# Kernel optimization log

Measured on AMD Instinct MI355X. Metric: run time of the kernel, lower is better.

## Reference

```python
import jax, jax.numpy as jnp
import numpy as np

B, T, C, H = 2, 2048, 1024, 16
D = C // H  # head dim = 64
EPS = 1e-5


def setup_inputs() -> dict:
    key = jax.random.key(0)
    k1, k2, k3 = jax.random.split(key, 3)
    x = jax.random.normal(k1, (B, T, C), dtype=jnp.float32)
    W_attn = jax.random.normal(k2, (3 * C, C), dtype=jnp.float32) * 0.02
    W_proj = jax.random.normal(k3, (C, C), dtype=jnp.float32) * 0.02
    # standard RoPE inverse frequencies, one per rotation pair (D//2)
    rope_freqs = 1.0 / (10000.0 ** (jnp.arange(D // 2, dtype=jnp.float32) * 2.0 / D))
    ln_weight = jnp.ones((C,), dtype=jnp.float32)
    ln_bias = jnp.zeros((C,), dtype=jnp.float32)
    return {"x": x, "rope_freqs": rope_freqs, "W_attn": W_attn,
            "W_proj": W_proj, "ln_weight": ln_weight, "ln_bias": ln_bias}


def _apply_rope(q, k, freqs):
    # q,k: [B,H,S,D]; matches torch apply_rope: split even/odd, concat halves
    S = q.shape[-2]
    theta = jnp.arange(S, dtype=q.dtype)[:, None] * freqs[None, :]  # [S, D/2]
    sin_t, cos_t = jnp.sin(theta), jnp.cos(theta)

    def rot(t):
        t1, t2 = t[..., 0::2], t[..., 1::2]
        return jnp.concatenate([t1 * cos_t - t2 * sin_t,
                                t1 * sin_t + t2 * cos_t], axis=-1)

    return rot(q), rot(k)


def reference(x, rope_freqs, W_attn, W_proj, ln_weight, ln_bias):
    Bv, Tv, Cv = x.shape
    qkv = x @ W_attn.T                      # [B,T,3C] (F.linear, no bias)
    q, k, v = jnp.split(qkv, 3, axis=-1)
    resh = lambda t: t.reshape(Bv, Tv, H, D).transpose(0, 2, 1, 3)  # [B,H,T,D]
    q, k, v = resh(q), resh(k), resh(v)
    q, k = _apply_rope(q, k, rope_freqs)
    scale = 1.0 / jnp.sqrt(jnp.asarray(D, dtype=x.dtype))
    scores = jnp.einsum('bhqd,bhkd->bhqk', q, k) * scale
    causal = jnp.tril(jnp.ones((Tv, Tv), dtype=bool))
    scores = jnp.where(causal[None, None], scores, -jnp.inf)
    att = jax.nn.softmax(scores, axis=-1)
    y = jnp.einsum('bhqk,bhkd->bhqd', att, v)
    y = y.transpose(0, 2, 1, 3).reshape(Bv, Tv, Cv)
    y = y @ W_proj.T                        # c_proj (bias=False)
    # resid dropout is identity in eval; LayerNorm (eps=1e-5, biased var)
    mean = jnp.mean(y, axis=-1, keepdims=True)
    var = jnp.mean(jnp.square(y - mean), axis=-1, keepdims=True)
    return (y - mean) / jnp.sqrt(var + EPS) * ln_weight + ln_bias
```

## Files before the change

### kernel.cpp

```cpp
#include <hip/hip_runtime.h>
#include <hip/hip_bf16.h>
#include <math.h>

typedef short bf16x8 __attribute__((ext_vector_type(8)));
typedef float f32x4 __attribute__((ext_vector_type(4)));

#define T_SEQ 2048
#define C_DIM 1024
#define H_HEADS 16
#define D_HEAD 64
#define BT 4096
#define C3 3072
#define BH 32

static __device__ inline unsigned short bf_bits(float f) {
    __hip_bfloat16 h = __float2bfloat16(f);
    unsigned short u;
    __builtin_memcpy(&u, &h, 2);
    return u;
}

static __device__ inline unsigned int cvtpk(float lo, float hi) {
    unsigned int r;
    asm("v_cvt_pk_bf16_f32 %0, %1, %2" : "=v"(r) : "v"(lo), "v"(hi));
    return r;
}

__device__ __forceinline__ void gload16(const void* g, void* l) {
    __builtin_amdgcn_global_load_lds(
        (const __attribute__((address_space(1))) void*)g,
        (__attribute__((address_space(3))) void*)l, 16, 0, 0);
}

__device__ __forceinline__ int swz(int r) {
    return ((((r & 3) ^ ((r >> 3) & 3)) | (((r >> 3) & 1) << 2)) << 3);
}

__global__ void cast_f32_bf16(const float* __restrict__ in,
                              __hip_bfloat16* __restrict__ out, int n4) {
    int i = blockIdx.x * blockDim.x + threadIdx.x;
    if (i >= n4) return;
    float4 v = reinterpret_cast<const float4*>(in)[i];
    ushort4 o;
    o.x = bf_bits(v.x); o.y = bf_bits(v.y); o.z = bf_bits(v.z); o.w = bf_bits(v.w);
    reinterpret_cast<ushort4*>(out)[i] = o;
}

__global__ void rope_table(const float* __restrict__ freqs, float2* __restrict__ tab) {
    int idx = blockIdx.x * 256 + threadIdx.x;
    int i = idx & 31, tp = idx >> 5;
    float th = (float)tp * freqs[i];
    tab[idx] = make_float2(cosf(th), sinf(th));
}

template<int MODE, int BN>
__global__ __launch_bounds__(256) void gemm_bt(
    const __hip_bfloat16* __restrict__ A,
    const __hip_bfloat16* __restrict__ Bw,
    void* __restrict__ Cout, int M, int N, int K,
    const float2* __restrict__ tab,
    __hip_bfloat16* __restrict__ q_s,
    __hip_bfloat16* __restrict__ k_s,
    __hip_bfloat16* __restrict__ v_t) {
    __shared__ __hip_bfloat16 As[128][64];
    __shared__ __hip_bfloat16 Bs[BN][64];
    const int t = threadIdx.x;
    const int lane = t & 63, w = t >> 6;
    const int wr = w >> 1, wc = w & 1;
    const int l15 = lane & 15, lg = lane >> 4;
    const int m0 = blockIdx.y * 128, n0 = blockIdx.x * BN;

    const int srow = lane >> 3;
    const int scol = ((lane & 7) ^ srow) * 8;
    const int xr = (l15 & 7) << 3;

    constexpr int NF = BN / 32;
    f32x4 acc[4][NF];
    f32x4 zero4 = {0.f, 0.f, 0.f, 0.f};
#pragma unroll
    for (int m = 0; m < 4; m++)
#pragma unroll
        for (int n = 0; n < NF; n++) acc[m][n] = zero4;

    const int nt = K >> 6;
    for (int tk = 0; tk < nt; tk++) {
        const int k0 = tk << 6;
#pragma unroll
        for (int i = 0; i < 4; i++) {
            int rbase = w * 32 + i * 8;
            gload16(&A[(size_t)(m0 + rbase + srow) * K + k0 + scol], &As[rbase][0]);
        }
#pragma unroll
        for (int i = 0; i < NF; i++) {
            int rbase = w * (BN / 4) + i * 8;
            gload16(&Bw[(size_t)(n0 + rbase + srow) * K + k0 + scol], &Bs[rbase][0]);
        }
        __syncthreads();
#pragma unroll
        for (int kk = 0; kk < 2; kk++) {
            bf16x8 a[4], b[NF];
            const int co = (kk * 32 + lg * 8) ^ xr;
#pragma unroll
            for (int m = 0; m < 4; m++)
                a[m] = *reinterpret_cast<const bf16x8*>(&As[wr * 64 + m * 16 + l15][co]);
#pragma unroll
            for (int n = 0; n < NF; n++)
                b[n] = *reinterpret_cast<const bf16x8*>(&Bs[wc * (BN / 2) + n * 16 + l15][co]);
            __builtin_amdgcn_s_setprio(1);
#pragma unroll
            for (int m = 0; m < 4; m++)
#pragma unroll
                for (int n = 0; n < NF; n++)
                    acc[m][n] = __builtin_amdgcn_mfma_f32_16x16x32_bf16(a[m], b[n], acc[m][n], 0, 0, 0);
            __builtin_amdgcn_s_setprio(0);
        }
        __syncthreads();
    }

    if (MODE == 2) {
        const int region = n0 >> 10;
#pragma unroll
        for (int m = 0; m < 4; m++)
#pragma unroll
            for (int n = 0; n < NF; n++) {
                const int col = n0 + wc * (BN / 2) + n * 16 + l15;
                const int d = col & 63;
                const int h = (col >> 6) & 15;
                const int row0 = m0 + wr * 64 + m * 16 + lg * 4;
                const int b = row0 >> 11;
                const int tp0 = row0 & 2047;
                if (region < 2) {
                    const int i = d >> 1, odd = d & 1;
                    const int dp = (d >> 1) + (odd ? 32 : 0);
                    __hip_bfloat16* dst = (region == 0) ? q_s : k_s;
                    const float sc = (region == 0) ? 0.125f * 1.44269504f : 1.0f;
#pragma unroll
                    for (int jj = 0; jj < 4; jj++) {
                        float own = acc[m][n][jj];
                        float par = __shfl_xor(own, 1);
                        float2 cs = tab[(tp0 + jj) * 32 + i];
                        float val = own * cs.x + (odd ? par : -par) * cs.y;
                        dst[((size_t)(b * H_HEADS + h) * T_SEQ + tp0 + jj) * D_HEAD + dp] =
                            __float2bfloat16(val * sc);
                    }
                } else {
                    ushort4 ov;
                    ov.x = bf_bits(acc[m][n][0]);
                    ov.y = bf_bits(acc[m][n][1]);
                    ov.z = bf_bits(acc[m][n][2]);
                    ov.w = bf_bits(acc[m][n][3]);
                    *reinterpret_cast<ushort4*>(
                        &v_t[((size_t)(b * H_HEADS + h) * D_HEAD + d) * T_SEQ + tp0]) = ov;
                }
            }
        return;
    }

#pragma unroll
    for (int m = 0; m < 4; m++)
#pragma unroll
        for (int n = 0; n < NF; n++)
#pragma unroll
            for (int jj = 0; jj < 4; jj++) {
                int row = m0 + wr * 64 + m * 16 + lg * 4 + jj;
                int col = n0 + wc * (BN / 2) + n * 16 + l15;
                float v = acc[m][n][jj];
                if (MODE == 1)
                    ((__hip_bfloat16*)Cout)[(size_t)row * N + col] = __float2bfloat16(v);
                else
                    ((float*)Cout)[(size_t)row * N + col] = v;
            }
}

__global__ __launch_bounds__(256, 4) void attn_kernel(
    const __hip_bfloat16* __restrict__ q_s,
    const __hip_bfloat16* __restrict__ k_s,
    const __hip_bfloat16* __restrict__ v_t,
    __hip_bfloat16* __restrict__ y) {
    __shared__ ushort Kbuf[2][64 * 64];
    __shared__ ushort Vbuf[2][64 * 64];

    const int bid = blockIdx.x;
    const int qt = 31 - (bid >> 5);
    const int bh = bid & 31;
    const int t = threadIdx.x, lane = t & 63, w = t >> 6;
    const int l15 = lane & 15, lg = lane >> 4;
    const size_t hbase = (size_t)bh * T_SEQ * D_HEAD;
    const int qr = qt * 64 + w * 16 + l15;

    bf16x8 aq[2];
#pragma unroll
    for (int dd = 0; dd < 2; dd++)
        aq[dd] = *reinterpret_cast<const bf16x8*>(&q_s[hbase + (size_t)qr * 64 + dd * 32 + lg * 8]);

    bf16x8 ones;
#pragma unroll
    for (int i = 0; i < 8; i++) ones[i] = (short)0x3F80;

    f32x4 zero4 = {0.f, 0.f, 0.f, 0.f};
    f32x4 o[4];
#pragma unroll
    for (int dc = 0; dc < 4; dc++) o[dc] = zero4;
    f32x4 lacc = zero4;
    float mr = -INFINITY;

    int koff[4][2], voff[4][2];
#pragma unroll
    for (int c = 0; c < 4; c++) {
        int kro = ((c >> 1) << 5) + ((c & 1) << 2) + ((l15 >> 2) << 3) + (l15 & 3);
        int sz = swz(kro);
#pragma unroll
        for (int dd = 0; dd < 2; dd++)
            koff[c][dd] = kro * 64 + ((dd * 32 + lg * 8) ^ sz);
    }
#pragma unroll
    for (int dc = 0; dc < 4; dc++) {
        int vro = dc * 16 + l15;
        int sz = swz(vro);
#pragma unroll
        for (int dd = 0; dd < 2; dd++)
            voff[dc][dd] = vro * 64 + ((dd * 32 + lg * 8) ^ sz);
    }

    const int srow = t >> 3;
    const int sgr = t & 7;

    auto stageKV = [&](int buf, int kbase) {
#pragma unroll
        for (int i = 0; i < 2; i++) {
            int r = i * 32 + srow;
            int gsw = (sgr ^ (swz(r) >> 3)) * 8;
            gload16(&k_s[hbase + (size_t)(kbase + r) * 64 + gsw],
                    &Kbuf[buf][(i * 32 + w * 8) * 64]);
            gload16(&v_t[hbase + (size_t)r * T_SEQ + kbase + gsw],
                    &Vbuf[buf][(i * 32 + w * 8) * 64]);
        }
    };

    int cur = 0;
    stageKV(0, 0);
    __syncthreads();

    for (int kt = 0; kt <= qt; kt++) {
        const int kt64 = kt << 6;
        if (kt < qt) stageKV(cur ^ 1, kt64 + 64);

        const ushort* Kc = Kbuf[cur];
        const ushort* Vc = Vbuf[cur];
        bf16x8 kf[4][2], av[4][2];
#pragma unroll
        for (int c = 0; c < 4; c++)
#pragma unroll
            for (int dd = 0; dd < 2; dd++)
                kf[c][dd] = *reinterpret_cast<const bf16x8*>(&Kc[koff[c][dd]]);
#pragma unroll
        for (int dc = 0; dc < 4; dc++)
#pragma unroll
            for (int dd = 0; dd < 2; dd++)
                av[dc][dd] = *reinterpret_cast<const bf16x8*>(&Vc[voff[dc][dd]]);

        f32x4 st[4];
        __builtin_amdgcn_s_setprio(1);
#pragma unroll
        for (int c = 0; c < 4; c++) {
            st[c] = zero4;
#pragma unroll
            for (int dd = 0; dd < 2; dd++)
                st[c] = __builtin_amdgcn_mfma_f32_16x16x32_bf16(kf[c][dd], aq[dd], st[c], 0, 0, 0);
        }
        __builtin_amdgcn_s_setprio(0);

        if (kt == qt) {
#pragma unroll
            for (int c = 0; c < 4; c++) {
                int kb = kt64 + ((c >> 1) << 5) + ((c & 1) << 2) + lg * 8;
#pragma unroll
                for (int jj = 0; jj < 4; jj++)
                    if (kb + jj > qr) st[c][jj] = -INFINITY;
            }
        }

        float m0a = fmaxf(st[0][0], st[0][1]), m0b = fmaxf(st[0][2], st[0][3]);
        float m1a = fmaxf(st[1][0], st[1][1]), m1b = fmaxf(st[1][2], st[1][3]);
        float m2a = fmaxf(st[2][0], st[2][1]), m2b = fmaxf(st[2][2], st[2][3]);
        float m3a = fmaxf(st[3][0], st[3][1]), m3b = fmaxf(st[3][2], st[3][3]);
        float lmx = fmaxf(fmaxf(fmaxf(m0a, m0b), fmaxf(m1a, m1b)),
                          fmaxf(fmaxf(m2a, m2b), fmaxf(m3a, m3b)));

        if (__any(lmx - mr > 8.f)) {
            float mx = fmaxf(lmx, __shfl_xor(lmx, 16));
            mx = fmaxf(mx, __shfl_xor(mx, 32));
            float mnew = fmaxf(mr, mx);
            float scl = __builtin_amdgcn_exp2f(mr - mnew);
            mr = mnew;
            lacc[0] *= scl;
#pragma unroll
            for (int dc = 0; dc < 4; dc++)
#pragma unroll
                for (int jj = 0; jj < 4; jj++) o[dc][jj] *= scl;
        }

#pragma unroll
        for (int c = 0; c < 4; c++)
#pragma unroll
            for (int jj = 0; jj < 4; jj++)
                st[c][jj] = __builtin_amdgcn_exp2f(st[c][jj] - mr);

        union { bf16x8 v; unsigned int u[4]; } pf0, pf1;
        pf0.u[0] = cvtpk(st[0][0], st[0][1]);
        pf0.u[1] = cvtpk(st[0][2], st[0][3]);
        pf0.u[2] = cvtpk(st[1][0], st[1][1]);
        pf0.u[3] = cvtpk(st[1][2], st[1][3]);
        pf1.u[0] = cvtpk(st[2][0], st[2][1]);
        pf1.u[1] = cvtpk(st[2][2], st[2][3]);
        pf1.u[2] = cvtpk(st[3][0], st[3][1]);
        pf1.u[3] = cvtpk(st[3][2], st[3][3]);

        __builtin_amdgcn_s_setprio(1);
        lacc = __builtin_amdgcn_mfma_f32_16x16x32_bf16(ones, pf0.v, lacc, 0, 0, 0);
        lacc = __builtin_amdgcn_mfma_f32_16x16x32_bf16(ones, pf1.v, lacc, 0, 0, 0);
#pragma unroll
        for (int dc = 0; dc < 4; dc++) {
            o[dc] = __builtin_amdgcn_mfma_f32_16x16x32_bf16(av[dc][0], pf0.v, o[dc], 0, 0, 0);
            o[dc] = __builtin_amdgcn_mfma_f32_16x16x32_bf16(av[dc][1], pf1.v, o[dc], 0, 0, 0);
        }
        __builtin_amdgcn_s_setprio(0);

        __syncthreads();
        cur ^= 1;
    }

    const int b = bh >> 4, h = bh & 15;
    float inv = 1.f / lacc[0];
#pragma unroll
    for (int dc = 0; dc < 4; dc++) {
        ushort4 ov;
        ov.x = bf_bits(o[dc][0] * inv);
        ov.y = bf_bits(o[dc][1] * inv);
        ov.z = bf_bits(o[dc][2] * inv);
        ov.w = bf_bits(o[dc][3] * inv);
        *reinterpret_cast<ushort4*>(
            &y[(size_t)(b * T_SEQ + qr) * C_DIM + h * 64 + dc * 16 + lg * 4]) = ov;
    }
}

__global__ __launch_bounds__(256) void ln_kernel(const __hip_bfloat16* __restrict__ y2,
                                                 const float* __restrict__ wgt,
                                                 const float* __restrict__ bias,
                                                 float* __restrict__ out) {
    const int row = blockIdx.x;
    const int t = threadIdx.x;
    ushort4 u = reinterpret_cast<const ushort4*>(y2 + (size_t)row * C_DIM)[t];
    float4 v;
    v.x = __bfloat162float(*(__hip_bfloat16*)&u.x);
    v.y = __bfloat162float(*(__hip_bfloat16*)&u.y);
    v.z = __bfloat162float(*(__hip_bfloat16*)&u.z);
    v.w = __bfloat162float(*(__hip_bfloat16*)&u.w);
    float s = v.x + v.y + v.z + v.w;
    float s2 = v.x * v.x + v.y * v.y + v.z * v.z + v.w * v.w;
#pragma unroll
    for (int d = 1; d < 64; d <<= 1) {
        s += __shfl_xor(s, d);
        s2 += __shfl_xor(s2, d);
    }
    __shared__ float ps[4], ps2[4];
    const int lane = t & 63, w = t >> 6;
    if (lane == 0) { ps[w] = s; ps2[w] = s2; }
    __syncthreads();
    s = ps[0] + ps[1] + ps[2] + ps[3];
    s2 = ps2[0] + ps2[1] + ps2[2] + ps2[3];
    float mean = s * (1.f / C_DIM);
    float var = s2 * (1.f / C_DIM) - mean * mean;
    float inv = rsqrtf(var + 1e-5f);
    float4 wv = reinterpret_cast<const float4*>(wgt)[t];
    float4 bv = reinterpret_cast<const float4*>(bias)[t];
    float4 ov;
    ov.x = (v.x - mean) * inv * wv.x + bv.x;
    ov.y = (v.y - mean) * inv * wv.y + bv.y;
    ov.z = (v.z - mean) * inv * wv.z + bv.z;
    ov.w = (v.w - mean) * inv * wv.w + bv.w;
    reinterpret_cast<float4*>(out + (size_t)row * C_DIM)[t] = ov;
}

extern "C" void kernel_launch(void* const* d_in, const int* in_sizes, int n_in,
                              void* d_out, int out_size, void* d_ws, size_t ws_size,
                              hipStream_t stream) {
    const float* x      = (const float*)d_in[0];
    const float* freqs  = (const float*)d_in[1];
    const float* W_attn = (const float*)d_in[2];
    const float* W_proj = (const float*)d_in[3];
    const float* lnw    = (const float*)d_in[4];
    const float* lnb    = (const float*)d_in[5];
    float* out = (float*)d_out;
    char* ws = (char*)d_ws;

    __hip_bfloat16* xb   = (__hip_bfloat16*)(ws);
    __hip_bfloat16* Wab  = (__hip_bfloat16*)(ws + 8388608);
    __hip_bfloat16* Wpb  = (__hip_bfloat16*)(ws + 14680064);
    float2*         tab  = (float2*)(ws + 16777216);
    __hip_bfloat16* q_s  = (__hip_bfloat16*)(ws + 41943040);
    __hip_bfloat16* k_s  = (__hip_bfloat16*)(ws + 50331648);
    __hip_bfloat16* v_t  = (__hip_bfloat16*)(ws + 58720256);
    __hip_bfloat16* y_at = (__hip_bfloat16*)(ws + 67108864);
    __hip_bfloat16* y2b  = (__hip_bfloat16*)(ws + 75497472);

    rope_table<<<(T_SEQ * 32) / 256, 256, 0, stream>>>(freqs, tab);
    cast_f32_bf16<<<(BT * C_DIM / 4) / 256, 256, 0, stream>>>(x, xb, BT * C_DIM / 4);
    cast_f32_bf16<<<(C3 * C_DIM / 4) / 256, 256, 0, stream>>>(W_attn, Wab, C3 * C_DIM / 4);
    cast_f32_bf16<<<(C_DIM * C_DIM / 4) / 256, 256, 0, stream>>>(W_proj, Wpb, C_DIM * C_DIM / 4);

    gemm_bt<2, 128><<<dim3(C3 / 128, BT / 128), 256, 0, stream>>>(
        xb, Wab, nullptr, BT, C3, C_DIM, tab, q_s, k_s, v_t);

    attn_kernel<<<1024, 256, 0, stream>>>(q_s, k_s, v_t, y_at);

    gemm_bt<1, 64><<<dim3(C_DIM / 64, BT / 128), 256, 0, stream>>>(
        y_at, Wpb, y2b, BT, C_DIM, C_DIM, nullptr, nullptr, nullptr, nullptr);

    ln_kernel<<<BT, 256, 0, stream>>>(y2b, lnw, lnb, out);
}
```

Baseline: 112.5 us.

## Use 128-row query tiles in attention and fuse prep kernels into one launch

The attention kernel moves to 512-thread blocks covering 128 query rows, so eight waves share each staged K/V tile. Waves whose rows lie entirely before the current key tile skip its compute, and the causal mask is applied only on tiles that cross the diagonal. The four setup launches (three casts and the RoPE table) are merged into one prep kernel to cut launch overhead. The trade-off is causal load imbalance inside a block, since early-row waves idle while later waves work, plus half as many blocks to fill the GPU.

After: 112.6 us. Within noise of the previous version (+0.1%).

```diff
diff --git a/kernel.cpp b/kernel.cpp
--- a/kernel.cpp
+++ b/kernel.cpp
@@ -36,21 +36,32 @@
     return ((((r & 3) ^ ((r >> 3) & 3)) | (((r >> 3) & 1) << 2)) << 3);
 }
 
-__global__ void cast_f32_bf16(const float* __restrict__ in,
-                              __hip_bfloat16* __restrict__ out, int n4) {
-    int i = blockIdx.x * blockDim.x + threadIdx.x;
-    if (i >= n4) return;
-    float4 v = reinterpret_cast<const float4*>(in)[i];
-    ushort4 o;
-    o.x = bf_bits(v.x); o.y = bf_bits(v.y); o.z = bf_bits(v.z); o.w = bf_bits(v.w);
-    reinterpret_cast<ushort4*>(out)[i] = o;
-}
-
-__global__ void rope_table(const float* __restrict__ freqs, float2* __restrict__ tab) {
-    int idx = blockIdx.x * 256 + threadIdx.x;
-    int i = idx & 31, tp = idx >> 5;
-    float th = (float)tp * freqs[i];
-    tab[idx] = make_float2(cosf(th), sinf(th));
+__global__ void prep_kernel(const float* __restrict__ x,
+                            const float* __restrict__ Wa,
+                            const float* __restrict__ Wp,
+                            const float* __restrict__ freqs,
+                            __hip_bfloat16* __restrict__ xb,
+                            __hip_bfloat16* __restrict__ Wab,
+                            __hip_bfloat16* __restrict__ Wpb,
+                            float2* __restrict__ tab) {
+    const int bidx = blockIdx.x, tid = threadIdx.x;
+    if (bidx < 8192) {
+        const float* src;
+        __hip_bfloat16* dst;
+        int i;
+        if (bidx < 4096)      { src = x;  dst = xb;  i = bidx * 256 + tid; }
+        else if (bidx < 7168) { src = Wa; dst = Wab; i = (bidx - 4096) * 256 + tid; }
+        else                  { src = Wp; dst = Wpb; i = (bidx - 7168) * 256 + tid; }
+        float4 v = reinterpret_cast<const float4*>(src)[i];
+        ushort4 o;
+        o.x = bf_bits(v.x); o.y = bf_bits(v.y); o.z = bf_bits(v.z); o.w = bf_bits(v.w);
+        reinterpret_cast<ushort4*>(dst)[i] = o;
+    } else {
+        int idx = (bidx - 8192) * 256 + tid;
+        int i = idx & 31, tp = idx >> 5;
+        float th = (float)tp * freqs[i];
+        tab[idx] = make_float2(cosf(th), sinf(th));
+    }
 }
 
 template<int MODE, int BN>
@@ -164,15 +175,11 @@
             for (int jj = 0; jj < 4; jj++) {
                 int row = m0 + wr * 64 + m * 16 + lg * 4 + jj;
                 int col = n0 + wc * (BN / 2) + n * 16 + l15;
-                float v = acc[m][n][jj];
-                if (MODE == 1)
-                    ((__hip_bfloat16*)Cout)[(size_t)row * N + col] = __float2bfloat16(v);
-                else
-                    ((float*)Cout)[(size_t)row * N + col] = v;
-            }
-}
-
-__global__ __launch_bounds__(256, 4) void attn_kernel(
+                ((__hip_bfloat16*)Cout)[(size_t)row * N + col] = __float2bfloat16(acc[m][n][jj]);
+            }
+}
+
+__global__ __launch_bounds__(512, 4) void attn_kernel(
     const __hip_bfloat16* __restrict__ q_s,
     const __hip_bfloat16* __restrict__ k_s,
     const __hip_bfloat16* __restrict__ v_t,
@@ -181,12 +188,13 @@
     __shared__ ushort Vbuf[2][64 * 64];
 
     const int bid = blockIdx.x;
-    const int qt = 31 - (bid >> 5);
+    const int qt = 15 - (bid >> 5);
     const int bh = bid & 31;
     const int t = threadIdx.x, lane = t & 63, w = t >> 6;
     const int l15 = lane & 15, lg = lane >> 4;
     const size_t hbase = (size_t)bh * T_SEQ * D_HEAD;
-    const int qr = qt * 64 + w * 16 + l15;
+    const int qrow0 = qt * 128 + w * 16;
+    const int qr = qrow0 + l15;
 
     bf16x8 aq[2];
 #pragma unroll
@@ -224,107 +232,105 @@
 
     const int srow = t >> 3;
     const int sgr = t & 7;
+    const int gsw = (sgr ^ (swz(srow) >> 3)) * 8;
 
     auto stageKV = [&](int buf, int kbase) {
-#pragma unroll
-        for (int i = 0; i < 2; i++) {
-            int r = i * 32 + srow;
-            int gsw = (sgr ^ (swz(r) >> 3)) * 8;
-            gload16(&k_s[hbase + (size_t)(kbase + r) * 64 + gsw],
-                    &Kbuf[buf][(i * 32 + w * 8) * 64]);
-            gload16(&v_t[hbase + (size_t)r * T_SEQ + kbase + gsw],
-                    &Vbuf[buf][(i * 32 + w * 8) * 64]);
-        }
+        gload16(&k_s[hbase + (size_t)(kbase + srow) * 64 + gsw], &Kbuf[buf][(w * 8) * 64]);
+        gload16(&v_t[hbase + (size_t)srow * T_SEQ + kbase + gsw], &Vbuf[buf][(w * 8) * 64]);
     };
 
     int cur = 0;
     stageKV(0, 0);
     __syncthreads();
 
-    for (int kt = 0; kt <= qt; kt++) {
+    const int last = 2 * qt + 1;
+    for (int kt = 0; kt <= last; kt++) {
         const int kt64 = kt << 6;
-        if (kt < qt) stageKV(cur ^ 1, kt64 + 64);
-
-        const ushort* Kc = Kbuf[cur];
-        const ushort* Vc = Vbuf[cur];
-        bf16x8 kf[4][2], av[4][2];
-#pragma unroll
-        for (int c = 0; c < 4; c++)
-#pragma unroll
-            for (int dd = 0; dd < 2; dd++)
-                kf[c][dd] = *reinterpret_cast<const bf16x8*>(&Kc[koff[c][dd]]);
-#pragma unroll
-        for (int dc = 0; dc < 4; dc++)
-#pragma unroll
-            for (int dd = 0; dd < 2; dd++)
-                av[dc][dd] = *reinterpret_cast<const bf16x8*>(&Vc[voff[dc][dd]]);
-
-        f32x4 st[4];
-        __builtin_amdgcn_s_setprio(1);
-#pragma unroll
-        for (int c = 0; c < 4; c++) {
-            st[c] = zero4;
-#pragma unroll
-            for (int dd = 0; dd < 2; dd++)
-                st[c] = __builtin_amdgcn_mfma_f32_16x16x32_bf16(kf[c][dd], aq[dd], st[c], 0, 0, 0);
+        if (kt < last) stageKV(cur ^ 1, kt64 + 64);
+
+        const bool live = (kt64 <= qrow0 + 15);
+        if (live) {
+            const ushort* Kc = Kbuf[cur];
+            const ushort* Vc = Vbuf[cur];
+            bf16x8 kf[4][2], av[4][2];
+#pragma unroll
+            for (int c = 0; c < 4; c++)
+#pragma unroll
+                for (int dd = 0; dd < 2; dd++)
+                    kf[c][dd] = *reinterpret_cast<const bf16x8*>(&Kc[koff[c][dd]]);
+#pragma unroll
+            for (int dc = 0; dc < 4; dc++)
+#pragma unroll
+                for (int dd = 0; dd < 2; dd++)
+                    av[dc][dd] = *reinterpret_cast<const bf16x8*>(&Vc[voff[dc][dd]]);
+
+            f32x4 st[4];
+            __builtin_amdgcn_s_setprio(1);
+#pragma unroll
+            for (int c = 0; c < 4; c++) {
+                st[c] = zero4;
+#pragma unroll
+                for (int dd = 0; dd < 2; dd++)
+                    st[c] = __builtin_amdgcn_mfma_f32_16x16x32_bf16(kf[c][dd], aq[dd], st[c], 0, 0, 0);
+            }
+            __builtin_amdgcn_s_setprio(0);
+
+            if (kt64 + 63 > qrow0) {
+#pragma unroll
+                for (int c = 0; c < 4; c++) {
+                    int kb = kt64 + ((c >> 1) << 5) + ((c & 1) << 2) + lg * 8;
+#pragma unroll
+                    for (int jj = 0; jj < 4; jj++)
+                        if (kb + jj > qr) st[c][jj] = -INFINITY;
+                }
+            }
+
+            float m0a = fmaxf(st[0][0], st[0][1]), m0b = fmaxf(st[0][2], st[0][3]);
+            float m1a = fmaxf(st[1][0], st[1][1]), m1b = fmaxf(st[1][2], st[1][3]);
+            float m2a = fmaxf(st[2][0], st[2][1]), m2b = fmaxf(st[2][2], st[2][3]);
+            float m3a = fmaxf(st[3][0], st[3][1]), m3b = fmaxf(st[3][2], st[3][3]);
+            float lmx = fmaxf(fmaxf(fmaxf(m0a, m0b), fmaxf(m1a, m1b)),
+                              fmaxf(fmaxf(m2a, m2b), fmaxf(m3a, m3b)));
+
+            if (__any(lmx - mr > 8.f)) {
+                float mx = fmaxf(lmx, __shfl_xor(lmx, 16));
+                mx = fmaxf(mx, __shfl_xor(mx, 32));
+                float mnew = fmaxf(mr, mx);
+                float scl = __builtin_amdgcn_exp2f(mr - mnew);
+                mr = mnew;
+                lacc[0] *= scl;
+#pragma unroll
+                for (int dc = 0; dc < 4; dc++)
+#pragma unroll
+                    for (int jj = 0; jj < 4; jj++) o[dc][jj] *= scl;
+            }
+
+#pragma unroll
+            for (int c = 0; c < 4; c++)
+#pragma unroll
+                for (int jj = 0; jj < 4; jj++)
+                    st[c][jj] = __builtin_amdgcn_exp2f(st[c][jj] - mr);
+
+            union { bf16x8 v; unsigned int u[4]; } pf0, pf1;
+            pf0.u[0] = cvtpk(st[0][0], st[0][1]);
+            pf0.u[1] = cvtpk(st[0][2], st[0][3]);
+            pf0.u[2] = cvtpk(st[1][0], st[1][1]);
+            pf0.u[3] = cvtpk(st[1][2], st[1][3]);
+            pf1.u[0] = cvtpk(st[2][0], st[2][1]);
+            pf1.u[1] = cvtpk(st[2][2], st[2][3]);
+            pf1.u[2] = cvtpk(st[3][0], st[3][1]);
+            pf1.u[3] = cvtpk(st[3][2], st[3][3]);
+
+            __builtin_amdgcn_s_setprio(1);
+            lacc = __builtin_amdgcn_mfma_f32_16x16x32_bf16(ones, pf0.v, lacc, 0, 0, 0);
+            lacc = __builtin_amdgcn_mfma_f32_16x16x32_bf16(ones, pf1.v, lacc, 0, 0, 0);
+#pragma unroll
+            for (int dc = 0; dc < 4; dc++) {
+                o[dc] = __builtin_amdgcn_mfma_f32_16x16x32_bf16(av[dc][0], pf0.v, o[dc], 0, 0, 0);
+                o[dc] = __builtin_amdgcn_mfma_f32_16x16x32_bf16(av[dc][1], pf1.v, o[dc], 0, 0, 0);
+            }
+            __builtin_amdgcn_s_setprio(0);
         }
-        __builtin_amdgcn_s_setprio(0);
-
-        if (kt == qt) {
-#pragma unroll
-            for (int c = 0; c < 4; c++) {
-                int kb = kt64 + ((c >> 1) << 5) + ((c & 1) << 2) + lg * 8;
-#pragma unroll
-                for (int jj = 0; jj < 4; jj++)
-                    if (kb + jj > qr) st[c][jj] = -INFINITY;
-            }
-        }
-
-        float m0a = fmaxf(st[0][0], st[0][1]), m0b = fmaxf(st[0][2], st[0][3]);
-        float m1a = fmaxf(st[1][0], st[1][1]), m1b = fmaxf(st[1][2], st[1][3]);
-        float m2a = fmaxf(st[2][0], st[2][1]), m2b = fmaxf(st[2][2], st[2][3]);
-        float m3a = fmaxf(st[3][0], st[3][1]), m3b = fmaxf(st[3][2], st[3][3]);
-        float lmx = fmaxf(fmaxf(fmaxf(m0a, m0b), fmaxf(m1a, m1b)),
-                          fmaxf(fmaxf(m2a, m2b), fmaxf(m3a, m3b)));
-
-        if (__any(lmx - mr > 8.f)) {
-            float mx = fmaxf(lmx, __shfl_xor(lmx, 16));
-            mx = fmaxf(mx, __shfl_xor(mx, 32));
-            float mnew = fmaxf(mr, mx);
-            float scl = __builtin_amdgcn_exp2f(mr - mnew);
-            mr = mnew;
-            lacc[0] *= scl;
-#pragma unroll
-            for (int dc = 0; dc < 4; dc++)
-#pragma unroll
-                for (int jj = 0; jj < 4; jj++) o[dc][jj] *= scl;
-        }
-
-#pragma unroll
-        for (int c = 0; c < 4; c++)
-#pragma unroll
-            for (int jj = 0; jj < 4; jj++)
-                st[c][jj] = __builtin_amdgcn_exp2f(st[c][jj] - mr);
-
-        union { bf16x8 v; unsigned int u[4]; } pf0, pf1;
-        pf0.u[0] = cvtpk(st[0][0], st[0][1]);
-        pf0.u[1] = cvtpk(st[0][2], st[0][3]);
-        pf0.u[2] = cvtpk(st[1][0], st[1][1]);
-        pf0.u[3] = cvtpk(st[1][2], st[1][3]);
-        pf1.u[0] = cvtpk(st[2][0], st[2][1]);
-        pf1.u[1] = cvtpk(st[2][2], st[2][3]);
-        pf1.u[2] = cvtpk(st[3][0], st[3][1]);
-        pf1.u[3] = cvtpk(st[3][2], st[3][3]);
-
-        __builtin_amdgcn_s_setprio(1);
-        lacc = __builtin_amdgcn_mfma_f32_16x16x32_bf16(ones, pf0.v, lacc, 0, 0, 0);
-        lacc = __builtin_amdgcn_mfma_f32_16x16x32_bf16(ones, pf1.v, lacc, 0, 0, 0);
-#pragma unroll
-        for (int dc = 0; dc < 4; dc++) {
-            o[dc] = __builtin_amdgcn_mfma_f32_16x16x32_bf16(av[dc][0], pf0.v, o[dc], 0, 0, 0);
-            o[dc] = __builtin_amdgcn_mfma_f32_16x16x32_bf16(av[dc][1], pf1.v, o[dc], 0, 0, 0);
-        }
-        __builtin_amdgcn_s_setprio(0);
 
         __syncthreads();
         cur ^= 1;
@@ -404,15 +410,12 @@
     __hip_bfloat16* y_at = (__hip_bfloat16*)(ws + 67108864);
     __hip_bfloat16* y2b  = (__hip_bfloat16*)(ws + 75497472);
 
-    rope_table<<<(T_SEQ * 32) / 256, 256, 0, stream>>>(freqs, tab);
-    cast_f32_bf16<<<(BT * C_DIM / 4) / 256, 256, 0, stream>>>(x, xb, BT * C_DIM / 4);
-    cast_f32_bf16<<<(C3 * C_DIM / 4) / 256, 256, 0, stream>>>(W_attn, Wab, C3 * C_DIM / 4);
-    cast_f32_bf16<<<(C_DIM * C_DIM / 4) / 256, 256, 0, stream>>>(W_proj, Wpb, C_DIM * C_DIM / 4);
+    prep_kernel<<<8448, 256, 0, stream>>>(x, W_attn, W_proj, freqs, xb, Wab, Wpb, tab);
 
     gemm_bt<2, 128><<<dim3(C3 / 128, BT / 128), 256, 0, stream>>>(
         xb, Wab, nullptr, BT, C3, C_DIM, tab, q_s, k_s, v_t);
 
-    attn_kernel<<<1024, 256, 0, stream>>>(q_s, k_s, v_t, y_at);
+    attn_kernel<<<512, 512, 0, stream>>>(q_s, k_s, v_t, y_at);
 
     gemm_bt<1, 64><<<dim3(C_DIM / 64, BT / 128), 256, 0, stream>>>(
         y_at, Wpb, y2b, BT, C_DIM, C_DIM, nullptr, nullptr, nullptr, nullptr);
```
